# Performance work log

Hardware: AMD Instinct MI355X
Metric: run time of the kernel (lower is better)

Reference implementation:

```python
import jax, jax.numpy as jnp
import numpy as np

N = 50000      # nodes per type
E = 800000     # edges per relation
D = 128        # input feature dim
H = 128        # hidden_channels


def setup_inputs() -> dict:
    key = jax.random.key(0)
    ks = jax.random.split(key, 20)
    f = lambda k, shp: jax.random.normal(k, shp, dtype=jnp.float32) * 0.05
    inp = {
        "x_ligand": jax.random.normal(ks[0], (N, D), dtype=jnp.float32),
        "x_protein": jax.random.normal(ks[1], (N, D), dtype=jnp.float32),
        "ei_lp": jax.random.randint(ks[2], (2, E), 0, N, dtype=jnp.int64),
        "ei_pp": jax.random.randint(ks[3], (2, E), 0, N, dtype=jnp.int64),
        "ei_ll": jax.random.randint(ks[4], (2, E), 0, N, dtype=jnp.int64),
        "Wl_lp": f(ks[5], (D, H)), "bl_lp": f(ks[6], (H,)), "Wr_lp": f(ks[7], (D, H)),
        "Wl_pp": f(ks[8], (D, H)), "bl_pp": f(ks[9], (H,)), "Wr_pp": f(ks[10], (D, H)),
        "Wl_ll": f(ks[11], (D, H)), "bl_ll": f(ks[12], (H,)), "Wr_ll": f(ks[13], (D, H)),
        "W_out": f(ks[14], (H, 1)), "b_out": f(ks[15], (1,)),
    }
    return inp


def _sage(x_src, x_dst, edge_index, Wl, bl, Wr):
    # PyG SAGEConv: mean-aggregate neighbor (src) features onto dst, then
    # out = lin_l(agg) + lin_r(x_dst)  (lin_l has bias, lin_r does not)
    src, dst = edge_index[0], edge_index[1]
    n_dst = x_dst.shape[0]
    msgs = x_src[src]                                      # [E, D] gather
    s = jax.ops.segment_sum(msgs, dst, num_segments=n_dst) # [N_dst, D]
    cnt = jax.ops.segment_sum(jnp.ones((edge_index.shape[1],), x_src.dtype),
                              dst, num_segments=n_dst)     # [N_dst]
    agg = s / jnp.maximum(cnt, 1.0)[:, None]               # mean, 0 if isolated
    return agg @ Wl + bl + x_dst @ Wr


def reference(x_ligand, x_protein, ei_lp, ei_pp, ei_ll,
              Wl_lp, bl_lp, Wr_lp, Wl_pp, bl_pp, Wr_pp,
              Wl_ll, bl_ll, Wr_ll, W_out, b_out):
    # HeteroConv: sum contributions per destination node type
    protein_out = (_sage(x_ligand, x_protein, ei_lp, Wl_lp, bl_lp, Wr_lp)
                   + _sage(x_protein, x_protein, ei_pp, Wl_pp, bl_pp, Wr_pp))
    ligand_out = _sage(x_ligand, x_ligand, ei_ll, Wl_ll, bl_ll, Wr_ll)
    # relu per node type; only ligand is used downstream
    lig = jax.nn.relu(ligand_out).mean(axis=0)             # [H]
    _ = jax.nn.relu(protein_out)                           # computed in original
    return lig @ W_out + b_out                             # [1]
```

## Files before the change

kernel.cpp:

```cpp
#include <hip/hip_runtime.h>
#include <hip/hip_bf16.h>

#define DIM 128
#define EPB 4096
#define NRBIN 1024
#define RCAP 1280

typedef __attribute__((ext_vector_type(8))) short bf16x8;
typedef __attribute__((ext_vector_type(4))) float f32x4;
typedef __attribute__((ext_vector_type(4))) short short4v;
typedef __attribute__((ext_vector_type(4))) int int4v;

__device__ inline unsigned short f2bf(float f) {
  union { float f; unsigned u; } v; v.f = f;
  return (unsigned short)((v.u + 0x7FFFu + ((v.u >> 16) & 1u)) >> 16);
}

__global__ __launch_bounds__(256) void prep_part_kernel(
    const int* __restrict__ ei, unsigned* __restrict__ chunkbuf,
    int* __restrict__ startsT, int* __restrict__ countsT, int E, int nchunk,
    const float* __restrict__ x, short* __restrict__ A,
    unsigned char* __restrict__ Xq,
    const float* __restrict__ Wl, const float* __restrict__ Wr,
    short* __restrict__ Bpack, int nnodes, int mpad, int xb) {
  __shared__ unsigned uns[EPB];
  __shared__ unsigned srt[EPB];
  __shared__ int lhist[NRBIN];
  __shared__ int lstart[NRBIN];
  __shared__ int tsum[256];
  const int tid = threadIdx.x;
  const int bid = blockIdx.x;

  if (bid >= nchunk) {
    if (bid < nchunk + xb) {
      int t = (bid - nchunk) * 256 + tid;
      int node = t >> 5;
      if (node >= mpad) return;
      int c = (t & 31) * 4;
      short4v o = (short4v){0, 0, 0, 0};
      unsigned q = 0;
      if (node < nnodes) {
        float4 v = *reinterpret_cast<const float4*>(x + (size_t)node * DIM + c);
        o.x = (short)f2bf(v.x); o.y = (short)f2bf(v.y);
        o.z = (short)f2bf(v.z); o.w = (short)f2bf(v.w);
        q = (unsigned)__builtin_amdgcn_cvt_pk_fp8_f32(v.x, v.y, 0, false);
        q = (unsigned)__builtin_amdgcn_cvt_pk_fp8_f32(v.z, v.w, (int)q, true);
      }
      *reinterpret_cast<short4v*>(A + (size_t)node * DIM + c) = o;
      *reinterpret_cast<unsigned*>(Xq + (size_t)node * DIM + c) = q;
    } else {
      int t = (bid - nchunk - xb) * 256 + tid;
      if (t >= 4096) return;
      int lane = t & 63, nt = (t >> 6) & 7, ks = t >> 9;
      int c = nt * 16 + (lane & 15);
      int kb = ks * 32 + ((lane >> 4) << 3);
      bf16x8 o;
#pragma unroll
      for (int j = 0; j < 8; ++j) {
        int k = kb + j;
        float v = (k < DIM) ? Wl[k * DIM + c] : Wr[(k - DIM) * DIM + c];
        o[j] = (short)f2bf(v);
      }
      reinterpret_cast<bf16x8*>(Bpack)[(ks * 8 + nt) * 64 + lane] = o;
    }
    return;
  }

  const int chunk = bid;
  const int base = chunk * EPB;
  const int count = min(EPB, E - base);

#pragma unroll
  for (int r = 0; r < NRBIN / 256; ++r) lhist[tid + 256 * r] = 0;
  __syncthreads();

  for (int r = 0; r < EPB / 1024; ++r) {
    int i = r * 1024 + tid * 4;
    if (i + 3 < count) {
      int4 s4 = *reinterpret_cast<const int4*>(ei + base + i);
      int4 d4 = *reinterpret_cast<const int4*>(ei + E + base + i);
      int ss[4] = {s4.x, s4.y, s4.z, s4.w};
      int dd[4] = {d4.x, d4.y, d4.z, d4.w};
#pragma unroll
      for (int k = 0; k < 4; ++k) {
        unsigned reg = (unsigned)dd[k] >> 6;
        uns[i + k] = (reg << 22) | ((unsigned)(dd[k] & 63) << 16) | (unsigned)ss[k];
        atomicAdd(&lhist[reg], 1);
      }
    } else {
      for (int k = 0; k < 4; ++k) {
        if (i + k < count) {
          int s = ei[base + i + k], d = ei[E + base + i + k];
          unsigned reg = (unsigned)d >> 6;
          uns[i + k] = (reg << 22) | ((unsigned)(d & 63) << 16) | (unsigned)s;
          atomicAdd(&lhist[reg], 1);
        }
      }
    }
  }
  __syncthreads();

  int h0 = lhist[tid * 4], h1 = lhist[tid * 4 + 1];
  int h2 = lhist[tid * 4 + 2], h3 = lhist[tid * 4 + 3];
  int local = h0 + h1 + h2 + h3;
  tsum[tid] = local;
  __syncthreads();
  for (int o = 1; o < 256; o <<= 1) {
    int t = (tid >= o) ? tsum[tid - o] : 0;
    __syncthreads();
    tsum[tid] += t;
    __syncthreads();
  }
  int tb = tsum[tid] - local;
  lstart[tid * 4]     = tb;
  lstart[tid * 4 + 1] = tb + h0;
  lstart[tid * 4 + 2] = tb + h0 + h1;
  lstart[tid * 4 + 3] = tb + h0 + h1 + h2;
  lhist[tid * 4] = 0; lhist[tid * 4 + 1] = 0;
  lhist[tid * 4 + 2] = 0; lhist[tid * 4 + 3] = 0;
  __syncthreads();

  for (int i = tid; i < count; i += 256) {
    unsigned e = uns[i];
    unsigned reg = e >> 22;
    int pos = lstart[reg] + atomicAdd(&lhist[reg], 1);
    srt[pos] = e;
  }
  __syncthreads();

  for (int r = 0; r < EPB / 1024; ++r) {
    int i = r * 1024 + tid * 4;
    if (i + 3 < count) {
      int4v v = {(int)srt[i], (int)srt[i + 1], (int)srt[i + 2], (int)srt[i + 3]};
      *reinterpret_cast<int4v*>(chunkbuf + (size_t)chunk * EPB + i) = v;
    } else {
      for (int k = 0; k < 4; ++k)
        if (i + k < count) chunkbuf[(size_t)chunk * EPB + i + k] = srt[i + k];
    }
  }
  for (int r = tid; r < NRBIN; r += 256) {
    startsT[(size_t)chunk * NRBIN + r] = lstart[r];
    countsT[(size_t)chunk * NRBIN + r] = lhist[r];
  }
}

__global__ __launch_bounds__(256) void compact_kernel(
    const unsigned* __restrict__ chunkbuf, const int* __restrict__ startsT,
    const int* __restrict__ countsT, int nchunk, unsigned* __restrict__ csr,
    int* __restrict__ cnt, int* __restrict__ off) {
  __shared__ unsigned raw[RCAP];
  __shared__ unsigned srt[RCAP];
  __shared__ int h[64];
  __shared__ int start[64];
  __shared__ int tsum[256];
  const int region = blockIdx.x;
  const int tid = threadIdx.x;

  int cn = 0, st = 0;
  if (tid < nchunk) {
    cn = countsT[(size_t)tid * NRBIN + region];
    st = startsT[(size_t)tid * NRBIN + region];
  }
  tsum[tid] = cn;
  __syncthreads();
  for (int o = 1; o < 256; o <<= 1) {
    int t = (tid >= o) ? tsum[tid - o] : 0;
    __syncthreads();
    tsum[tid] += t;
    __syncthreads();
  }
  const int pfx = tsum[tid] - cn;
  int total = min(tsum[255], RCAP);

  const unsigned* src = chunkbuf + (size_t)tid * EPB + st;
  for (int j = 0; j < cn && pfx + j < RCAP; ++j) raw[pfx + j] = src[j];
  if (tid < 64) h[tid] = 0;
  __syncthreads();

  for (int i = tid; i < total; i += 256) atomicAdd(&h[(raw[i] >> 16) & 63], 1);
  __syncthreads();
  if (tid == 0) {
    int s = 0;
    for (int i = 0; i < 64; ++i) { start[i] = s; s += h[i]; }
  }
  __syncthreads();
  if (tid < 64) {
    int node = region * 64 + tid;
    cnt[node] = h[tid];
    off[node] = region * RCAP + start[tid];
    h[tid] = 0;
  }
  __syncthreads();
  for (int i = tid; i < total; i += 256) {
    unsigned e = raw[i];
    int d = (e >> 16) & 63;
    int pos = start[d] + atomicAdd(&h[d], 1);
    srt[pos] = e & 0xFFFFu;
  }
  __syncthreads();
  for (int i = tid; i < total; i += 256) csr[(size_t)region * RCAP + i] = srt[i];
}

__global__ __launch_bounds__(1024) void aggmm_kernel(
    const int* __restrict__ cnt, const int* __restrict__ off,
    const unsigned* __restrict__ bucket, const short* __restrict__ A,
    const unsigned char* __restrict__ Xq,
    const short* __restrict__ Bpack, const float* __restrict__ bl,
    float* __restrict__ partial, int nnodes) {
  __shared__ short a_lds[64 * 256];
  const int tid = threadIdx.x;
  const int wave = tid >> 6;
  const int lane = tid & 63;
  const int mt = blockIdx.x;
  const unsigned short* xq =
      reinterpret_cast<const unsigned short*>(Xq) + lane;

  const int nb = mt * 64 + wave * 4;
  int cv = 0, ov = 0;
  if (lane < 4 && nb + lane < nnodes) {
    cv = cnt[nb + lane];
    ov = off[nb + lane];
  }
  int degs[4], bases[4];
#pragma unroll
  for (int n = 0; n < 4; ++n) {
    degs[n]  = __builtin_amdgcn_readlane(cv, n);
    bases[n] = __builtin_amdgcn_readlane(ov, n);
  }
  unsigned ents[4];
#pragma unroll
  for (int n = 0; n < 4; ++n)
    ents[n] = (lane < degs[n]) ? bucket[bases[n] + lane] : 0u;

#pragma unroll
  for (int n = 0; n < 4; ++n) {
    const int row = wave * 4 + n;
    const int deg = degs[n];
    const int dcap = min(deg, 64);
    float l0 = 0.f, h0 = 0.f, l1 = 0.f, h1 = 0.f;
    int j = 0;
    for (; j + 15 < dcap; j += 16) {
      unsigned short u[16];
#pragma unroll
      for (int k = 0; k < 16; ++k) {
        int s = __builtin_amdgcn_readlane((int)ents[n], j + k);
        u[k] = xq[(size_t)s * 64];
      }
#pragma unroll
      for (int k = 0; k < 16; ++k) {
        float lo = __builtin_amdgcn_cvt_f32_fp8((int)(unsigned)u[k], 0);
        float hi = __builtin_amdgcn_cvt_f32_fp8((int)(unsigned)u[k], 1);
        if (k & 1) { l1 += lo; h1 += hi; }
        else       { l0 += lo; h0 += hi; }
      }
    }
    for (; j + 7 < dcap; j += 8) {
      unsigned short u[8];
#pragma unroll
      for (int k = 0; k < 8; ++k) {
        int s = __builtin_amdgcn_readlane((int)ents[n], j + k);
        u[k] = xq[(size_t)s * 64];
      }
#pragma unroll
      for (int k = 0; k < 8; ++k) {
        float lo = __builtin_amdgcn_cvt_f32_fp8((int)(unsigned)u[k], 0);
        float hi = __builtin_amdgcn_cvt_f32_fp8((int)(unsigned)u[k], 1);
        if (k & 1) { l1 += lo; h1 += hi; }
        else       { l0 += lo; h0 += hi; }
      }
    }
    for (; j < dcap; ++j) {
      int s = __builtin_amdgcn_readlane((int)ents[n], j);
      unsigned short u0 = xq[(size_t)s * 64];
      l0 += __builtin_amdgcn_cvt_f32_fp8((int)(unsigned)u0, 0);
      h0 += __builtin_amdgcn_cvt_f32_fp8((int)(unsigned)u0, 1);
    }
    for (; j < deg; ++j) {
      int s = __builtin_amdgcn_readfirstlane((int)bucket[bases[n] + j]);
      unsigned short u0 = xq[(size_t)s * 64];
      l0 += __builtin_amdgcn_cvt_f32_fp8((int)(unsigned)u0, 0);
      h0 += __builtin_amdgcn_cvt_f32_fp8((int)(unsigned)u0, 1);
    }
    const float r = (nb + n < nnodes) ? 1.0f / fmaxf((float)deg, 1.0f) : 0.f;
    const unsigned o = (unsigned)f2bf((l0) * r) |
                       ((unsigned)f2bf((h0) * r) << 16);
    const unsigned o2 = (unsigned)f2bf((l0 + l1) * r) |
                        ((unsigned)f2bf((h0 + h1) * r) << 16);
    (void)o;
    int byte = ((row * 512 + (lane >> 2) * 16) ^ ((row & 7) << 4)) + (lane & 3) * 4;
    *reinterpret_cast<unsigned*>(reinterpret_cast<char*>(a_lds) + byte) = o2;
  }

  {
    int row = tid >> 4;
    int kc = 16 + (tid & 15);
    bf16x8 v = *reinterpret_cast<const bf16x8*>(
        A + (size_t)(mt * 64 + row) * DIM + (kc - 16) * 8);
    int byte = (row * 512 + kc * 16) ^ ((row & 7) << 4);
    *reinterpret_cast<bf16x8*>(reinterpret_cast<char*>(a_lds) + byte) = v;
  }
  __syncthreads();

  f32x4 acc[2];
#pragma unroll
  for (int nt = 0; nt < 2; ++nt) acc[nt] = (f32x4){0.f, 0.f, 0.f, 0.f};

  const int stripe = wave >> 2;
  const int ntbase = (wave & 3) * 2;
  const int arow = stripe * 16 + (lane & 15);
  const int kgrp = lane >> 4;
  const bf16x8* Bp = reinterpret_cast<const bf16x8*>(Bpack);

#pragma unroll
  for (int ks = 0; ks < 8; ++ks) {
    int byte = (arow * 512 + (ks * 32 + kgrp * 8) * 2) ^ ((arow & 7) << 4);
    bf16x8 a = *reinterpret_cast<const bf16x8*>(reinterpret_cast<char*>(a_lds) + byte);
#pragma unroll
    for (int nt = 0; nt < 2; ++nt) {
      bf16x8 b = Bp[(ks * 8 + ntbase + nt) * 64 + lane];
      acc[nt] = __builtin_amdgcn_mfma_f32_16x16x32_bf16(a, b, acc[nt], 0, 0, 0);
    }
  }

  const int col16 = lane & 15;
  const int rowbase = mt * 64 + stripe * 16 + kgrp * 4;
#pragma unroll
  for (int nt = 0; nt < 2; ++nt) {
    const int c = (ntbase + nt) * 16 + col16;
    const float bb = bl[c];
    float s = 0.f;
#pragma unroll
    for (int rg = 0; rg < 4; ++rg) {
      float v = fmaxf(acc[nt][rg] + bb, 0.f);
      s += (rowbase + rg < nnodes) ? v : 0.f;
    }
    s += __shfl_xor(s, 16);
    s += __shfl_xor(s, 32);
    if (kgrp == 0) partial[((size_t)mt * 4 + stripe) * DIM + c] = s;
  }
}

__global__ __launch_bounds__(256) void red1_kernel(
    const float* __restrict__ partial, int nrows, float* __restrict__ red) {
  __shared__ float tmp[128];
  const int c = threadIdx.x & 127;
  const int half = threadIdx.x >> 7;
  const int chunk = (nrows + 127) / 128;
  const int r0 = blockIdx.x * chunk;
  const int r1 = min(r0 + chunk, nrows);
  float s = 0.f;
  for (int r = r0 + half; r < r1; r += 2) s += partial[(size_t)r * DIM + c];
  if (half) tmp[c] = s;
  __syncthreads();
  if (!half) red[(size_t)blockIdx.x * DIM + c] = s + tmp[c];
}

__global__ __launch_bounds__(256) void red2_kernel(
    const float* __restrict__ red, const float* __restrict__ Wout,
    const float* __restrict__ bout, float* __restrict__ out, int nnodes) {
  __shared__ float tmp[128];
  __shared__ float prod[128];
  const int c = threadIdx.x & 127;
  const int half = threadIdx.x >> 7;
  float s = 0.f;
  for (int r = half; r < 128; r += 2) s += red[(size_t)r * DIM + c];
  if (half) tmp[c] = s;
  __syncthreads();
  if (!half) prod[c] = (s + tmp[c]) * Wout[c];
  __syncthreads();
  if (threadIdx.x == 0) {
    float v = 0.f;
    for (int i = 0; i < 128; ++i) v += prod[i];
    out[0] = v / (float)nnodes + bout[0];
  }
}

extern "C" void kernel_launch(void* const* d_in, const int* in_sizes, int n_in,
                              void* d_out, int out_size, void* d_ws, size_t ws_size,
                              hipStream_t stream) {
  const float* x    = (const float*)d_in[0];
  const int*   ei   = (const int*)d_in[4];
  const float* Wl   = (const float*)d_in[11];
  const float* bl   = (const float*)d_in[12];
  const float* Wr   = (const float*)d_in[13];
  const float* Wout = (const float*)d_in[14];
  const float* bout = (const float*)d_in[15];

  const int nnodes = in_sizes[0] / DIM;
  const int E = in_sizes[4] / 2;
  const int mtiles = (nnodes + 63) / 64;
  const int mpad = mtiles * 64;
  const int nchunk = (E + EPB - 1) / EPB;

  unsigned*      chunkbuf = (unsigned*)d_ws;
  int*           startsT  = (int*)(chunkbuf + (size_t)nchunk * EPB);
  int*           countsT  = startsT + (size_t)nchunk * NRBIN;
  unsigned*      csr      = (unsigned*)(countsT + (size_t)nchunk * NRBIN);
  int*           cnt      = (int*)(csr + (size_t)mtiles * RCAP);
  int*           off      = cnt + mpad;
  short*         A        = (short*)(off + mpad);
  unsigned char* Xq       = (unsigned char*)(A + (size_t)mpad * DIM);
  short*         Bpack    = (short*)(Xq + (size_t)mpad * DIM);
  float*         red      = (float*)(Bpack + 32768);
  float*         partial  = (float*)chunkbuf;

  const int xb = mpad / 8;
  prep_part_kernel<<<nchunk + xb + 16, 256, 0, stream>>>(
      ei, chunkbuf, startsT, countsT, E, nchunk,
      x, A, Xq, Wl, Wr, Bpack, nnodes, mpad, xb);

  compact_kernel<<<mtiles, 256, 0, stream>>>(chunkbuf, startsT, countsT, nchunk,
                                             csr, cnt, off);

  aggmm_kernel<<<mtiles, 1024, 0, stream>>>(cnt, off, csr, A, Xq, Bpack, bl,
                                            partial, nnodes);

  red1_kernel<<<128, 256, 0, stream>>>(partial, mtiles * 4, red);
  red2_kernel<<<1, 256, 0, stream>>>(red, Wout, bout, (float*)d_out, nnodes);
}
```

Measured before the change: 85.58 us.

## Fuse CSR compaction into aggregation-matmul kernel using shared-memory neighbor lists

Removes the separate compact kernel and performs the per-region prefix sum, histogram and counting sort of edges inside the aggregation kernel. The neighbor lists go into LDS instead of a global CSR array. This drops one launch and a global write and re-read of the CSR, cnt and off arrays. In exchange the 1024-thread aggregation block runs the serial sort phase with most threads idle and uses more LDS per block, which may lower occupancy. The partial buffer is moved off chunkbuf because chunkbuf is now read in the same kernel.

```diff
diff --git a/kernel.cpp b/kernel.cpp
--- a/kernel.cpp
+++ b/kernel.cpp
@@ -144,106 +144,84 @@
   }
 }
 
-__global__ __launch_bounds__(256) void compact_kernel(
+__global__ __launch_bounds__(1024) void aggmm_kernel(
     const unsigned* __restrict__ chunkbuf, const int* __restrict__ startsT,
-    const int* __restrict__ countsT, int nchunk, unsigned* __restrict__ csr,
-    int* __restrict__ cnt, int* __restrict__ off) {
-  __shared__ unsigned raw[RCAP];
-  __shared__ unsigned srt[RCAP];
-  __shared__ int h[64];
-  __shared__ int start[64];
-  __shared__ int tsum[256];
-  const int region = blockIdx.x;
-  const int tid = threadIdx.x;
-
-  int cn = 0, st = 0;
-  if (tid < nchunk) {
-    cn = countsT[(size_t)tid * NRBIN + region];
-    st = startsT[(size_t)tid * NRBIN + region];
-  }
-  tsum[tid] = cn;
-  __syncthreads();
-  for (int o = 1; o < 256; o <<= 1) {
-    int t = (tid >= o) ? tsum[tid - o] : 0;
-    __syncthreads();
-    tsum[tid] += t;
-    __syncthreads();
-  }
-  const int pfx = tsum[tid] - cn;
-  int total = min(tsum[255], RCAP);
-
-  const unsigned* src = chunkbuf + (size_t)tid * EPB + st;
-  for (int j = 0; j < cn && pfx + j < RCAP; ++j) raw[pfx + j] = src[j];
-  if (tid < 64) h[tid] = 0;
-  __syncthreads();
-
-  for (int i = tid; i < total; i += 256) atomicAdd(&h[(raw[i] >> 16) & 63], 1);
-  __syncthreads();
-  if (tid == 0) {
-    int s = 0;
-    for (int i = 0; i < 64; ++i) { start[i] = s; s += h[i]; }
-  }
-  __syncthreads();
-  if (tid < 64) {
-    int node = region * 64 + tid;
-    cnt[node] = h[tid];
-    off[node] = region * RCAP + start[tid];
-    h[tid] = 0;
-  }
-  __syncthreads();
-  for (int i = tid; i < total; i += 256) {
-    unsigned e = raw[i];
-    int d = (e >> 16) & 63;
-    int pos = start[d] + atomicAdd(&h[d], 1);
-    srt[pos] = e & 0xFFFFu;
-  }
-  __syncthreads();
-  for (int i = tid; i < total; i += 256) csr[(size_t)region * RCAP + i] = srt[i];
-}
-
-__global__ __launch_bounds__(1024) void aggmm_kernel(
-    const int* __restrict__ cnt, const int* __restrict__ off,
-    const unsigned* __restrict__ bucket, const short* __restrict__ A,
-    const unsigned char* __restrict__ Xq,
+    const int* __restrict__ countsT, int nchunk,
+    const short* __restrict__ A, const unsigned char* __restrict__ Xq,
     const short* __restrict__ Bpack, const float* __restrict__ bl,
     float* __restrict__ partial, int nnodes) {
   __shared__ short a_lds[64 * 256];
+  __shared__ unsigned raw[RCAP];
+  __shared__ unsigned short slist[RCAP];
+  __shared__ int h[64];
+  __shared__ int deg_s[64];
+  __shared__ int st_s[64];
+  __shared__ int tsum[256];
   const int tid = threadIdx.x;
   const int wave = tid >> 6;
   const int lane = tid & 63;
   const int mt = blockIdx.x;
+
+  int cn = 0, st = 0;
+  if (tid < 256) {
+    if (tid < nchunk) {
+      cn = countsT[(size_t)tid * NRBIN + mt];
+      st = startsT[(size_t)tid * NRBIN + mt];
+    }
+    tsum[tid] = cn;
+  }
+  __syncthreads();
+  for (int o = 1; o < 256; o <<= 1) {
+    int t = (tid >= o && tid < 256) ? tsum[tid - o] : 0;
+    __syncthreads();
+    if (tid < 256) tsum[tid] += t;
+    __syncthreads();
+  }
+  const int total = min(tsum[255], RCAP);
+  if (tid < 256) {
+    const int pfx = tsum[tid] - cn;
+    const unsigned* src = chunkbuf + (size_t)tid * EPB + st;
+    for (int j = 0; j < cn && pfx + j < RCAP; ++j) raw[pfx + j] = src[j];
+  }
+  if (tid < 64) h[tid] = 0;
+  __syncthreads();
+
+  for (int i = tid; i < total; i += 1024) atomicAdd(&h[(raw[i] >> 16) & 63], 1);
+  __syncthreads();
+  if (tid == 0) {
+    int s = 0;
+    for (int i = 0; i < 64; ++i) { st_s[i] = s; s += h[i]; }
+  }
+  __syncthreads();
+  if (tid < 64) { deg_s[tid] = h[tid]; h[tid] = 0; }
+  __syncthreads();
+  for (int i = tid; i < total; i += 1024) {
+    unsigned e = raw[i];
+    int d = (e >> 16) & 63;
+    int pos = st_s[d] + atomicAdd(&h[d], 1);
+    slist[pos] = (unsigned short)(e & 0xFFFFu);
+  }
+  __syncthreads();
+
   const unsigned short* xq =
       reinterpret_cast<const unsigned short*>(Xq) + lane;
-
   const int nb = mt * 64 + wave * 4;
-  int cv = 0, ov = 0;
-  if (lane < 4 && nb + lane < nnodes) {
-    cv = cnt[nb + lane];
-    ov = off[nb + lane];
-  }
-  int degs[4], bases[4];
-#pragma unroll
-  for (int n = 0; n < 4; ++n) {
-    degs[n]  = __builtin_amdgcn_readlane(cv, n);
-    bases[n] = __builtin_amdgcn_readlane(ov, n);
-  }
-  unsigned ents[4];
-#pragma unroll
-  for (int n = 0; n < 4; ++n)
-    ents[n] = (lane < degs[n]) ? bucket[bases[n] + lane] : 0u;
 
 #pragma unroll
   for (int n = 0; n < 4; ++n) {
     const int row = wave * 4 + n;
-    const int deg = degs[n];
+    const bool live = (nb + n < nnodes);
+    const int deg = live ? deg_s[row] : 0;
+    const int base = st_s[row];
     const int dcap = min(deg, 64);
+    unsigned ent = (lane < dcap) ? (unsigned)slist[base + lane] : 0u;
     float l0 = 0.f, h0 = 0.f, l1 = 0.f, h1 = 0.f;
     int j = 0;
     for (; j + 15 < dcap; j += 16) {
       unsigned short u[16];
 #pragma unroll
       for (int k = 0; k < 16; ++k) {
-        int s = __builtin_amdgcn_readlane((int)ents[n], j + k);
+        int s = __builtin_amdgcn_readlane((int)ent, j + k);
         u[k] = xq[(size_t)s * 64];
       }
 #pragma unroll
@@ -258,7 +236,7 @@
       unsigned short u[8];
 #pragma unroll
       for (int k = 0; k < 8; ++k) {
-        int s = __builtin_amdgcn_readlane((int)ents[n], j + k);
+        int s = __builtin_amdgcn_readlane((int)ent, j + k);
         u[k] = xq[(size_t)s * 64];
       }
 #pragma unroll
@@ -270,25 +248,22 @@
       }
     }
     for (; j < dcap; ++j) {
-      int s = __builtin_amdgcn_readlane((int)ents[n], j);
+      int s = __builtin_amdgcn_readlane((int)ent, j);
       unsigned short u0 = xq[(size_t)s * 64];
       l0 += __builtin_amdgcn_cvt_f32_fp8((int)(unsigned)u0, 0);
       h0 += __builtin_amdgcn_cvt_f32_fp8((int)(unsigned)u0, 1);
     }
     for (; j < deg; ++j) {
-      int s = __builtin_amdgcn_readfirstlane((int)bucket[bases[n] + j]);
+      int s = (int)slist[base + j];
       unsigned short u0 = xq[(size_t)s * 64];
       l0 += __builtin_amdgcn_cvt_f32_fp8((int)(unsigned)u0, 0);
       h0 += __builtin_amdgcn_cvt_f32_fp8((int)(unsigned)u0, 1);
     }
-    const float r = (nb + n < nnodes) ? 1.0f / fmaxf((float)deg, 1.0f) : 0.f;
-    const unsigned o = (unsigned)f2bf((l0) * r) |
-                       ((unsigned)f2bf((h0) * r) << 16);
-    const unsigned o2 = (unsigned)f2bf((l0 + l1) * r) |
-                        ((unsigned)f2bf((h0 + h1) * r) << 16);
-    (void)o;
+    const float r = live ? 1.0f / fmaxf((float)deg, 1.0f) : 0.f;
+    const unsigned o = (unsigned)f2bf((l0 + l1) * r) |
+                       ((unsigned)f2bf((h0 + h1) * r) << 16);
     int byte = ((row * 512 + (lane >> 2) * 16) ^ ((row & 7) << 4)) + (lane & 3) * 4;
-    *reinterpret_cast<unsigned*>(reinterpret_cast<char*>(a_lds) + byte) = o2;
+    *reinterpret_cast<unsigned*>(reinterpret_cast<char*>(a_lds) + byte) = o;
   }
 
   {
@@ -395,25 +370,19 @@
   unsigned*      chunkbuf = (unsigned*)d_ws;
   int*           startsT  = (int*)(chunkbuf + (size_t)nchunk * EPB);
   int*           countsT  = startsT + (size_t)nchunk * NRBIN;
-  unsigned*      csr      = (unsigned*)(countsT + (size_t)nchunk * NRBIN);
-  int*           cnt      = (int*)(csr + (size_t)mtiles * RCAP);
-  int*           off      = cnt + mpad;
-  short*         A        = (short*)(off + mpad);
+  short*         A        = (short*)(countsT + (size_t)nchunk * NRBIN);
   unsigned char* Xq       = (unsigned char*)(A + (size_t)mpad * DIM);
   short*         Bpack    = (short*)(Xq + (size_t)mpad * DIM);
   float*         red      = (float*)(Bpack + 32768);
-  float*         partial  = (float*)chunkbuf;
+  float*         partial  = red + 128 * 128;
 
   const int xb = mpad / 8;
   prep_part_kernel<<<nchunk + xb + 16, 256, 0, stream>>>(
       ei, chunkbuf, startsT, countsT, E, nchunk,
       x, A, Xq, Wl, Wr, Bpack, nnodes, mpad, xb);
 
-  compact_kernel<<<mtiles, 256, 0, stream>>>(chunkbuf, startsT, countsT, nchunk,
-                                             csr, cnt, off);
-
-  aggmm_kernel<<<mtiles, 1024, 0, stream>>>(cnt, off, csr, A, Xq, Bpack, bl,
-                                            partial, nnodes);
+  aggmm_kernel<<<mtiles, 1024, 0, stream>>>(chunkbuf, startsT, countsT, nchunk,
+                                            A, Xq, Bpack, bl, partial, nnodes);
 
   red1_kernel<<<128, 256, 0, stream>>>(partial, mtiles * 4, red);
   red2_kernel<<<1, 256, 0, stream>>>(red, Wout, bout, (float*)d_out, nnodes);
```

New measurement: 108.4 us. +26.7%, slower.
